# Performance work log

Measured on AMD Instinct MI355X. Metric: run time of the kernel, lower is better.

The kernel has to match this reference:

```python
import jax, jax.numpy as jnp
import numpy as np

NUM_EMBEDDINGS = 1024
EMBEDDING_DIM = 256
COMMITMENT_COST = 0.25
EPS_NORM = 1e-12  # F.normalize eps


def _l2_normalize(x, axis=-1):
    n = jnp.sqrt(jnp.sum(x * x, axis=axis, keepdims=True))
    return x / jnp.maximum(n, EPS_NORM)


def setup_inputs() -> dict:
    key = jax.random.key(0)
    k_in, k_w = jax.random.split(key)
    inputs = jax.random.normal(k_in, (16, 2048, 256), dtype=jnp.float32)
    # nn.Embedding weight initialized uniform(-1/K, 1/K)
    weight = jax.random.uniform(
        k_w, (NUM_EMBEDDINGS, EMBEDDING_DIM), dtype=jnp.float32,
        minval=-1.0 / NUM_EMBEDDINGS, maxval=1.0 / NUM_EMBEDDINGS)
    return {"inputs": inputs, "weight": weight}


def reference(inputs, weight):
    # inputs: [B, T, D]  weight: [K, D]
    B, T, D = inputs.shape
    K = weight.shape[0]

    x = jax.lax.stop_gradient(inputs)
    # cosine distance: normalized dot products  [B, T, K]
    distances = jnp.einsum(
        "btd,kd->btk", _l2_normalize(x), _l2_normalize(weight))

    encoding_indices = jnp.argmax(distances, axis=-1)            # [B, T]
    encodings = jax.nn.one_hot(encoding_indices, K, dtype=jnp.float32)  # [B, T, K]

    # one-hot matmul with codebook == gather
    quantized = jnp.take(weight, encoding_indices, axis=0)       # [B, T, D]

    e_latent_loss = COMMITMENT_COST * jnp.mean(
        (jax.lax.stop_gradient(quantized) - inputs) ** 2)
    q_latent_loss = jnp.mean((quantized - x) ** 2)

    # straight-through estimator
    quantized_st = inputs + jax.lax.stop_gradient(quantized - inputs)

    avg_probs = jnp.mean(encodings, axis=0)                      # [T, K]
    perplexity = jnp.exp(-jnp.sum(avg_probs * jnp.log(avg_probs + 1e-10)))

    # eval path (3D input): contra_loss = 0.0, no EMA/anchor update
    return (quantized_st,
            encoding_indices[..., None],
            q_latent_loss,
            e_latent_loss,
            perplexity,
            encodings)
```

## Files before the change

### kernel.cpp

```cpp
#include <hip/hip_runtime.h>
#include <math.h>
#include <float.h>

#define NUM_EMB   1024
#define DIM       256
#define BATCH     16
#define TLEN      2048
#define NTOK      (BATCH * TLEN)
#define QUANT_N   (NTOK * DIM)

#define QUANT_OFF 0
#define IDX_OFF   QUANT_N
#define QLOSS_OFF (IDX_OFF + NTOK)
#define ELOSS_OFF (QLOSS_OFF + 1)
#define PERP_OFF  (QLOSS_OFF + 2)
#define ENC_OFF   (QLOSS_OFF + 3)

typedef _Float16 f16;
typedef f16   f16x4 __attribute__((ext_vector_type(4)));
typedef f16   f16x8 __attribute__((ext_vector_type(8)));
typedef float f32x4 __attribute__((ext_vector_type(4)));

#define WS_XS_BYTE      0u
#define WS_WSP_BYTE     33554432u
#define WS_CNT_BYTE     34603008u
#define WS_WIN_BYTE     42991616u
#define WS_ACC_BYTE     43253760u
#define WS_NEED         (43253760u + 64u)

#define LWS_WHAT_BYTE   0
#define LWS_CNT_BYTE    1048576
#define LWS_ACC_BYTE    9437184

__device__ __forceinline__ void gl2lds16(const void* g, void* l) {
    __builtin_amdgcn_global_load_lds(
        (const __attribute__((address_space(1))) void*)g,
        (__attribute__((address_space(3))) void*)l, 16, 0, 0);
}


__global__ void k_zero_big(int4* __restrict__ counts4, int4* __restrict__ win4,
                           double* __restrict__ acc) {
    int i = blockIdx.x * blockDim.x + threadIdx.x;
    if (i < 524288) counts4[i] = make_int4(0, 0, 0, 0);
    else            win4[i - 524288] = make_int4(0, 0, 0, 0);
    if (i == 0) { acc[0] = 0.0; acc[1] = 0.0; }
}

__global__ void k_split_x(const float4* __restrict__ x4, f16* __restrict__ Xs) {
    int i = blockIdx.x * 256 + threadIdx.x;
    int row = i >> 6;
    int c4  = i & 63;
    float4 v = x4[i];
    f16 h0 = (f16)v.x, h1 = (f16)v.y, h2 = (f16)v.z, h3 = (f16)v.w;
    f16 l0 = (f16)(v.x - (float)h0), l1 = (f16)(v.y - (float)h1);
    f16 l2 = (f16)(v.z - (float)h2), l3 = (f16)(v.w - (float)h3);
    f16x4 hv = {h0, h1, h2, h3}, lv = {l0, l1, l2, l3};
    *(f16x4*)&Xs[(size_t)row * 512 + c4 * 4]       = hv;
    *(f16x4*)&Xs[(size_t)row * 512 + 256 + c4 * 4] = lv;
}

__global__ void k_norm_w_split(const float* __restrict__ w, f16* __restrict__ Ws) {
    int k = blockIdx.x;
    int lane = threadIdx.x;
    float4 v = ((const float4*)(w + (size_t)k * DIM))[lane];
    float ss = v.x * v.x + v.y * v.y + v.z * v.z + v.w * v.w;
    #pragma unroll
    for (int off = 32; off > 0; off >>= 1) ss += __shfl_down(ss, off);
    ss = __shfl(ss, 0);
    float denom = fmaxf(sqrtf(ss), 1e-12f);
    float a = v.x / denom, b = v.y / denom, c = v.z / denom, d = v.w / denom;
    f16 h0 = (f16)a, h1 = (f16)b, h2 = (f16)c, h3 = (f16)d;
    f16 l0 = (f16)(a - (float)h0), l1 = (f16)(b - (float)h1);
    f16 l2 = (f16)(c - (float)h2), l3 = (f16)(d - (float)h3);
    f16x4 hv = {h0, h1, h2, h3}, lv = {l0, l1, l2, l3};
    *(f16x4*)&Ws[(size_t)k * 512 + lane * 4]       = hv;
    *(f16x4*)&Ws[(size_t)k * 512 + 256 + lane * 4] = lv;
}

__global__ __launch_bounds__(256)
void k_gemm(const f16* __restrict__ Xs,
            const f16* __restrict__ Ws,
            unsigned long long* __restrict__ winners)
{
    __shared__ f16 As[128 * 64];
    __shared__ f16 Bs[128 * 64];

    const int tid  = threadIdx.x;
    const int w    = tid >> 6, lane = tid & 63;
    const int tb   = blockIdx.x & 255;
    const int pg   = blockIdx.x >> 8;
    const int tok0 = tb * 128;
    const int cw0  = pg * 128;
    const int wr   = w >> 1, wc = w & 1;
    const int quad = lane >> 4, l16 = lane & 15;

    const char* Xb = (const char*)Xs + (size_t)tok0 * 1024;
    const char* Wb = (const char*)Ws + (size_t)cw0 * 1024;

    int srow[4], sgpart[4];
    #pragma unroll
    for (int j = 0; j < 4; ++j) {
        int c = (w * 4 + j) * 64 + lane;
        srow[j]   = c >> 3;
        sgpart[j] = ((c & 7) ^ ((c >> 3) & 7)) * 16;
    }

    f32x4 acc[4][4];
    #pragma unroll
    for (int mi = 0; mi < 4; ++mi)
        #pragma unroll
        for (int ni = 0; ni < 4; ++ni)
            acc[mi][ni] = (f32x4){0.f, 0.f, 0.f, 0.f};

    for (int ks = 0; ks < 12; ++ks) {
        const int g = ks >> 2, r = ks & 3;
        const int akoff = ((g == 2) ? 512 : 0) + r * 128;
        const int bkoff = ((g == 1) ? 512 : 0) + r * 128;
        __syncthreads();
        #pragma unroll
        for (int j = 0; j < 4; ++j) {
            gl2lds16(Xb + (size_t)srow[j] * 1024 + akoff + sgpart[j],
                     (char*)As + (w * 4 + j) * 1024);
            gl2lds16(Wb + (size_t)srow[j] * 1024 + bkoff + sgpart[j],
                     (char*)Bs + (w * 4 + j) * 1024);
        }
        __syncthreads();

        #pragma unroll
        for (int ksub = 0; ksub < 2; ++ksub) {
            f16x8 af[4], bf[4];
            #pragma unroll
            for (int mi = 0; mi < 4; ++mi) {
                const int m = wr * 64 + mi * 16 + l16;
                const int slot = (quad + ksub * 4) ^ (l16 & 7);
                af[mi] = *(const f16x8*)&As[m * 64 + slot * 8];
            }
            #pragma unroll
            for (int ni = 0; ni < 4; ++ni) {
                const int n = wc * 64 + ni * 16 + l16;
                const int slot = (quad + ksub * 4) ^ (l16 & 7);
                bf[ni] = *(const f16x8*)&Bs[n * 64 + slot * 8];
            }
            #pragma unroll
            for (int mi = 0; mi < 4; ++mi)
                #pragma unroll
                for (int ni = 0; ni < 4; ++ni)
                    acc[mi][ni] = __builtin_amdgcn_mfma_f32_16x16x32_f16(
                        af[mi], bf[ni], acc[mi][ni], 0, 0, 0);
        }
    }

    #pragma unroll
    for (int mi = 0; mi < 4; ++mi) {
        #pragma unroll
        for (int rr = 0; rr < 4; ++rr) {
            float bv = acc[mi][0][rr];
            int   bk = cw0 + wc * 64 + l16;
            #pragma unroll
            for (int ni = 1; ni < 4; ++ni) {
                float v = acc[mi][ni][rr];
                int  kk = cw0 + wc * 64 + ni * 16 + l16;
                if (v > bv) { bv = v; bk = kk; }
            }
            unsigned int ub = __float_as_uint(bv);
            ub = (ub & 0x80000000u) ? ~ub : (ub | 0x80000000u);
            unsigned long long key =
                ((unsigned long long)ub << 32) | (unsigned int)(1023 - bk);
            #pragma unroll
            for (int msk = 1; msk < 16; msk <<= 1) {
                unsigned long long o = __shfl_xor(key, msk, 64);
                if (o > key) key = o;
            }
            if (l16 == mi * 4 + rr) {
                const int row = wr * 64 + mi * 16 + quad * 4 + rr;
                atomicMax(&winners[tok0 + row], key);
            }
        }
    }
}

__global__ __launch_bounds__(256)
void k_epilogue(const float* __restrict__ x, const float* __restrict__ w,
                const unsigned long long* __restrict__ winners,
                float* __restrict__ out, int* __restrict__ counts,
                double* __restrict__ acc)
{
    const int wv = threadIdx.x >> 6, lane = threadIdx.x & 63;
    const int base = blockIdx.x * 32 + wv * 8;
    float mse = 0.0f;
    for (int t = 0; t < 8; ++t) {
        const int n = base + t;
        const int idx = 1023 - (int)(winners[n] & 1023u);
        float4 wvv = *(const float4*)(w + (size_t)idx * DIM + lane * 4);
        float4 xv  = *(const float4*)(x + (size_t)n * DIM + lane * 4);
        float dx = wvv.x - xv.x, dy = wvv.y - xv.y, dz = wvv.z - xv.z, dw2 = wvv.w - xv.w;
        mse += dx * dx + dy * dy + dz * dz + dw2 * dw2;
        *(float4*)(out + QUANT_OFF + (size_t)n * DIM + lane * 4) = wvv;
        if (lane == 0) {
            out[IDX_OFF + n] = (float)idx;
            atomicAdd(&counts[(n & (TLEN - 1)) * NUM_EMB + idx], 1);
        }
        float* enc = out + ENC_OFF + (size_t)n * NUM_EMB;
        #pragma unroll
        for (int s = 0; s < 4; ++s) {
            int kbase = s * 256 + lane * 4;
            float4 e;
            e.x = (kbase + 0 == idx) ? 1.0f : 0.0f;
            e.y = (kbase + 1 == idx) ? 1.0f : 0.0f;
            e.z = (kbase + 2 == idx) ? 1.0f : 0.0f;
            e.w = (kbase + 3 == idx) ? 1.0f : 0.0f;
            *(float4*)(enc + kbase) = e;
        }
    }
    #pragma unroll
    for (int off = 32; off > 0; off >>= 1) mse += __shfl_down(mse, off);
    if (lane == 0) atomicAdd(&acc[0], (double)mse);
}

__global__ void k_entropy(const int* __restrict__ counts, double* __restrict__ acc) {
    const int tid = blockIdx.x * blockDim.x + threadIdx.x;
    const int stride = gridDim.x * blockDim.x;
    float s = 0.0f;
    for (int e = tid; e < TLEN * NUM_EMB; e += stride) {
        int c = counts[e];
        if (c > 0) {
            float p = (float)c * 0.0625f;
            s += p * logf(p + 1e-10f);
        }
    }
    #pragma unroll
    for (int off = 32; off > 0; off >>= 1) s += __shfl_down(s, off);
    __shared__ float wsum[4];
    int lane = threadIdx.x & 63, wave = threadIdx.x >> 6;
    if (lane == 0) wsum[wave] = s;
    __syncthreads();
    if (threadIdx.x == 0) atomicAdd(&acc[1], (double)(wsum[0] + wsum[1] + wsum[2] + wsum[3]));
}

__global__ void k_final(const double* __restrict__ acc, float* __restrict__ out) {
    float mse_mean = (float)(acc[0] / (double)QUANT_N);
    out[QLOSS_OFF] = mse_mean;
    out[ELOSS_OFF] = 0.25f * mse_mean;
    float arg = -(float)acc[1];
    out[PERP_OFF] = (arg < 87.0f) ? expf(arg) : 3.0e38f;
}

__global__ void k_zero_legacy(int4* __restrict__ counts4, double* __restrict__ acc) {
    int i = blockIdx.x * blockDim.x + threadIdx.x;
    counts4[i] = make_int4(0, 0, 0, 0);
    if (i == 0) { acc[0] = 0.0; acc[1] = 0.0; }
}

__global__ void k_norm_w_legacy(const float* __restrict__ w, float* __restrict__ w_hat) {
    int k = blockIdx.x, lane = threadIdx.x;
    float4 v = ((const float4*)(w + (size_t)k * DIM))[lane];
    float ss = v.x * v.x + v.y * v.y + v.z * v.z + v.w * v.w;
    #pragma unroll
    for (int off = 32; off > 0; off >>= 1) ss += __shfl_down(ss, off);
    ss = __shfl(ss, 0);
    float denom = fmaxf(sqrtf(ss), 1e-12f);
    float4 o = {v.x / denom, v.y / denom, v.z / denom, v.w / denom};
    ((float4*)(w_hat + (size_t)k * DIM))[lane] = o;
}

#define BK 16
#define LDP 132
__global__ __launch_bounds__(256)
void k_main_legacy(const float* __restrict__ x, const float* __restrict__ w,
                   const float* __restrict__ w_hat, float* __restrict__ out,
                   int* __restrict__ counts, double* __restrict__ acc)
{
    __shared__ float As[BK][LDP];
    __shared__ float Bs[BK][LDP];
    __shared__ float redV[128][17];
    __shared__ int   redK[128][17];
    __shared__ int   sIdx[128];

    const int tid  = threadIdx.x;
    const int tok0 = blockIdx.x * 128;
    const int tr   = tid >> 4, tc = tid & 15;
    float rbestV = -3.0e30f; int rbestK = 0;
    const int strow = tid >> 2, stdq = tid & 3;

    for (int panel = 0; panel < 8; ++panel) {
        const int cw0 = panel * 128;
        float accs[8][8];
        #pragma unroll
        for (int i = 0; i < 8; ++i)
            #pragma unroll
            for (int j = 0; j < 8; ++j) accs[i][j] = 0.0f;
        for (int d0 = 0; d0 < DIM; d0 += BK) {
            __syncthreads();
            #pragma unroll
            for (int it = 0; it < 2; ++it) {
                int r = strow + it * 64;
                float4 a = *(const float4*)(x + (size_t)(tok0 + r) * DIM + d0 + stdq * 4);
                float4 b = *(const float4*)(w_hat + (size_t)(cw0 + r) * DIM + d0 + stdq * 4);
                As[stdq * 4 + 0][r] = a.x; As[stdq * 4 + 1][r] = a.y;
                As[stdq * 4 + 2][r] = a.z; As[stdq * 4 + 3][r] = a.w;
                Bs[stdq * 4 + 0][r] = b.x; Bs[stdq * 4 + 1][r] = b.y;
                Bs[stdq * 4 + 2][r] = b.z; Bs[stdq * 4 + 3][r] = b.w;
            }
            __syncthreads();
            #pragma unroll
            for (int kk = 0; kk < BK; ++kk) {
                float4 a0 = *(const float4*)&As[kk][tr * 8];
                float4 a1 = *(const float4*)&As[kk][tr * 8 + 4];
                float4 b0 = *(const float4*)&Bs[kk][tc * 8];
                float4 b1 = *(const float4*)&Bs[kk][tc * 8 + 4];
                float af[8] = {a0.x, a0.y, a0.z, a0.w, a1.x, a1.y, a1.z, a1.w};
                float bf[8] = {b0.x, b0.y, b0.z, b0.w, b1.x, b1.y, b1.z, b1.w};
                #pragma unroll
                for (int i = 0; i < 8; ++i)
                    #pragma unroll
                    for (int j = 0; j < 8; ++j)
                        accs[i][j] = fmaf(af[i], bf[j], accs[i][j]);
            }
        }
        #pragma unroll
        for (int i = 0; i < 8; ++i) {
            float bv = accs[i][0]; int bj = 0;
            #pragma unroll
            for (int j = 1; j < 8; ++j)
                if (accs[i][j] > bv) { bv = accs[i][j]; bj = j; }
            redV[tr * 8 + i][tc] = bv;
            redK[tr * 8 + i][tc] = cw0 + tc * 8 + bj;
        }
        __syncthreads();
        if (tid < 128) {
            #pragma unroll
            for (int g = 0; g < 16; ++g) {
                float v = redV[tid][g]; int kk2 = redK[tid][g];
                if (v > rbestV || (v == rbestV && kk2 < rbestK)) { rbestV = v; rbestK = kk2; }
            }
        }
        __syncthreads();
    }
    if (tid < 128) sIdx[tid] = rbestK;
    __syncthreads();

    const int wave = tid >> 6, lane = tid & 63;
    float mse = 0.0f;
    for (int tl = wave * 32; tl < wave * 32 + 32; ++tl) {
        const int n = tok0 + tl;
        const int idx = sIdx[tl];
        float4 wv = *(const float4*)(w + (size_t)idx * DIM + lane * 4);
        float4 xv = *(const float4*)(x + (size_t)n * DIM + lane * 4);
        float dx = wv.x - xv.x, dy = wv.y - xv.y, dz = wv.z - xv.z, dww = wv.w - xv.w;
        mse += dx * dx + dy * dy + dz * dz + dww * dww;
        *(float4*)(out + QUANT_OFF + (size_t)n * DIM + lane * 4) = wv;
        if (lane == 0) {
            out[IDX_OFF + n] = (float)idx;
            atomicAdd(&counts[(n & (TLEN - 1)) * NUM_EMB + idx], 1);
        }
        float* enc = out + ENC_OFF + (size_t)n * NUM_EMB;
        #pragma unroll
        for (int s = 0; s < 4; ++s) {
            int kbase = s * 256 + lane * 4;
            float4 e;
            e.x = (kbase + 0 == idx) ? 1.0f : 0.0f;
            e.y = (kbase + 1 == idx) ? 1.0f : 0.0f;
            e.z = (kbase + 2 == idx) ? 1.0f : 0.0f;
            e.w = (kbase + 3 == idx) ? 1.0f : 0.0f;
            *(float4*)(enc + kbase) = e;
        }
    }
    #pragma unroll
    for (int off = 32; off > 0; off >>= 1) mse += __shfl_down(mse, off);
    if (lane == 0) atomicAdd(&acc[0], (double)mse);
}

extern "C" void kernel_launch(void* const* d_in, const int* in_sizes, int n_in,
                              void* d_out, int out_size, void* d_ws, size_t ws_size,
                              hipStream_t stream) {
    const float* x = (const float*)d_in[0];
    const float* w = (const float*)d_in[1];
    float* out = (float*)d_out;

    if (ws_size >= WS_NEED) {
        f16*    Xs      = (f16*)((char*)d_ws + WS_XS_BYTE);
        f16*    Wsp     = (f16*)((char*)d_ws + WS_WSP_BYTE);
        int*    counts  = (int*)((char*)d_ws + WS_CNT_BYTE);
        unsigned long long* winners = (unsigned long long*)((char*)d_ws + WS_WIN_BYTE);
        double* acc     = (double*)((char*)d_ws + WS_ACC_BYTE);

        k_zero_big<<<2112, 256, 0, stream>>>((int4*)counts, (int4*)winners, acc);
        k_split_x<<<8192, 256, 0, stream>>>((const float4*)x, Xs);
        k_norm_w_split<<<NUM_EMB, 64, 0, stream>>>(w, Wsp);
        k_gemm<<<2048, 256, 0, stream>>>(Xs, Wsp, winners);
        k_epilogue<<<1024, 256, 0, stream>>>(x, w, winners, out, counts, acc);
        k_entropy<<<512, 256, 0, stream>>>(counts, acc);
        k_final<<<1, 1, 0, stream>>>(acc, out);
    } else {
        float*  w_hat  = (float*)((char*)d_ws + LWS_WHAT_BYTE);
        int*    counts = (int*)((char*)d_ws + LWS_CNT_BYTE);
        double* acc    = (double*)((char*)d_ws + LWS_ACC_BYTE);

        k_zero_legacy<<<2048, 256, 0, stream>>>((int4*)counts, acc);
        k_norm_w_legacy<<<NUM_EMB, 64, 0, stream>>>(w, w_hat);
        k_main_legacy<<<NTOK / 128, 256, 0, stream>>>(x, w, w_hat, out, counts, acc);
        k_entropy<<<512, 256, 0, stream>>>(counts, acc);
        k_final<<<1, 1, 0, stream>>>(acc, out);
    }
}
```

Measured before the change: 335.6 us.

## Fuse prep kernels, double-buffer GEMM LDS, and fuse epilogue via last-block counter

Merges the zeroing, x split and codebook normalize kernels into one launch. The GEMM now double-buffers its LDS tiles so the next k-slice loads while the current one computes. The last of the 8 codebook-group blocks for each token tile, detected through an atomic tile counter, runs the gather, one-hot and loss epilogue inline, which removes a separate epilogue launch. The cost is doubled LDS per block, which can lower occupancy, plus a serialized tail on the last-arriving blocks.

```diff
diff --git a/kernel.cpp b/kernel.cpp
--- a/kernel.cpp
+++ b/kernel.cpp
@@ -26,7 +26,8 @@
 #define WS_CNT_BYTE     34603008u
 #define WS_WIN_BYTE     42991616u
 #define WS_ACC_BYTE     43253760u
-#define WS_NEED         (43253760u + 64u)
+#define WS_TC_BYTE      43253824u
+#define WS_NEED         43254848u
 
 #define LWS_WHAT_BYTE   0
 #define LWS_CNT_BYTE    1048576
@@ -39,127 +40,143 @@
 }
 
 
-__global__ void k_zero_big(int4* __restrict__ counts4, int4* __restrict__ win4,
-                           double* __restrict__ acc) {
-    int i = blockIdx.x * blockDim.x + threadIdx.x;
-    if (i < 524288) counts4[i] = make_int4(0, 0, 0, 0);
-    else            win4[i - 524288] = make_int4(0, 0, 0, 0);
-    if (i == 0) { acc[0] = 0.0; acc[1] = 0.0; }
-}
-
-__global__ void k_split_x(const float4* __restrict__ x4, f16* __restrict__ Xs) {
-    int i = blockIdx.x * 256 + threadIdx.x;
-    int row = i >> 6;
-    int c4  = i & 63;
-    float4 v = x4[i];
-    f16 h0 = (f16)v.x, h1 = (f16)v.y, h2 = (f16)v.z, h3 = (f16)v.w;
-    f16 l0 = (f16)(v.x - (float)h0), l1 = (f16)(v.y - (float)h1);
-    f16 l2 = (f16)(v.z - (float)h2), l3 = (f16)(v.w - (float)h3);
-    f16x4 hv = {h0, h1, h2, h3}, lv = {l0, l1, l2, l3};
-    *(f16x4*)&Xs[(size_t)row * 512 + c4 * 4]       = hv;
-    *(f16x4*)&Xs[(size_t)row * 512 + 256 + c4 * 4] = lv;
-}
-
-__global__ void k_norm_w_split(const float* __restrict__ w, f16* __restrict__ Ws) {
-    int k = blockIdx.x;
-    int lane = threadIdx.x;
-    float4 v = ((const float4*)(w + (size_t)k * DIM))[lane];
-    float ss = v.x * v.x + v.y * v.y + v.z * v.z + v.w * v.w;
-    #pragma unroll
-    for (int off = 32; off > 0; off >>= 1) ss += __shfl_down(ss, off);
-    ss = __shfl(ss, 0);
-    float denom = fmaxf(sqrtf(ss), 1e-12f);
-    float a = v.x / denom, b = v.y / denom, c = v.z / denom, d = v.w / denom;
-    f16 h0 = (f16)a, h1 = (f16)b, h2 = (f16)c, h3 = (f16)d;
-    f16 l0 = (f16)(a - (float)h0), l1 = (f16)(b - (float)h1);
-    f16 l2 = (f16)(c - (float)h2), l3 = (f16)(d - (float)h3);
-    f16x4 hv = {h0, h1, h2, h3}, lv = {l0, l1, l2, l3};
-    *(f16x4*)&Ws[(size_t)k * 512 + lane * 4]       = hv;
-    *(f16x4*)&Ws[(size_t)k * 512 + 256 + lane * 4] = lv;
+__global__ void k_prep(const float4* __restrict__ x4, f16* __restrict__ Xs,
+                       const float* __restrict__ w, f16* __restrict__ Ws,
+                       int4* __restrict__ counts4, int4* __restrict__ win4,
+                       int* __restrict__ tilecnt, double* __restrict__ acc)
+{
+    const int b = blockIdx.x, tid = threadIdx.x;
+    if (b < 8192) {
+        int i = b * 256 + tid;
+        int row = i >> 6, c4 = i & 63;
+        float4 v = x4[i];
+        f16 h0 = (f16)v.x, h1 = (f16)v.y, h2 = (f16)v.z, h3 = (f16)v.w;
+        f16 l0 = (f16)(v.x - (float)h0), l1 = (f16)(v.y - (float)h1);
+        f16 l2 = (f16)(v.z - (float)h2), l3 = (f16)(v.w - (float)h3);
+        f16x4 hv = {h0, h1, h2, h3}, lv = {l0, l1, l2, l3};
+        *(f16x4*)&Xs[(size_t)row * 512 + c4 * 4]       = hv;
+        *(f16x4*)&Xs[(size_t)row * 512 + 256 + c4 * 4] = lv;
+    } else if (b < 10240) {
+        counts4[(b - 8192) * 256 + tid] = make_int4(0, 0, 0, 0);
+    } else if (b < 10304) {
+        win4[(b - 10240) * 256 + tid] = make_int4(0, 0, 0, 0);
+    } else if (b < 10560) {
+        int k = (b - 10304) * 4 + (tid >> 6);
+        int lane = tid & 63;
+        float4 v = ((const float4*)(w + (size_t)k * DIM))[lane];
+        float ss = v.x * v.x + v.y * v.y + v.z * v.z + v.w * v.w;
+        #pragma unroll
+        for (int off = 32; off > 0; off >>= 1) ss += __shfl_down(ss, off);
+        ss = __shfl(ss, 0);
+        float denom = fmaxf(sqrtf(ss), 1e-12f);
+        float a = v.x / denom, bb = v.y / denom, c = v.z / denom, d = v.w / denom;
+        f16 h0 = (f16)a, h1 = (f16)bb, h2 = (f16)c, h3 = (f16)d;
+        f16 l0 = (f16)(a - (float)h0), l1 = (f16)(bb - (float)h1);
+        f16 l2 = (f16)(c - (float)h2), l3 = (f16)(d - (float)h3);
+        f16x4 hv = {h0, h1, h2, h3}, lv = {l0, l1, l2, l3};
+        *(f16x4*)&Ws[(size_t)k * 512 + lane * 4]       = hv;
+        *(f16x4*)&Ws[(size_t)k * 512 + 256 + lane * 4] = lv;
+    } else {
+        if (tid < 256) tilecnt[tid] = 0;
+        if (tid == 0) { acc[0] = 0.0; acc[1] = 0.0; }
+    }
 }
 
 __global__ __launch_bounds__(256)
 void k_gemm(const f16* __restrict__ Xs,
             const f16* __restrict__ Ws,
-            unsigned long long* __restrict__ winners)
+            const float* __restrict__ x, const float* __restrict__ w,
+            unsigned long long* __restrict__ winners,
+            int* __restrict__ counts, int* __restrict__ tilecnt,
+            float* __restrict__ out, double* __restrict__ acc)
 {
-    __shared__ f16 As[128 * 64];
-    __shared__ f16 Bs[128 * 64];
+    __shared__ f16 A0[8192];
+    __shared__ f16 B0[8192];
+    __shared__ f16 A1[8192];
+    __shared__ f16 B1[8192];
+    __shared__ int sLast;
 
     const int tid  = threadIdx.x;
-    const int w    = tid >> 6, lane = tid & 63;
+    const int wv   = tid >> 6, lane = tid & 63;
     const int tb   = blockIdx.x & 255;
     const int pg   = blockIdx.x >> 8;
     const int tok0 = tb * 128;
     const int cw0  = pg * 128;
-    const int wr   = w >> 1, wc = w & 1;
+    const int wr   = wv >> 1, wc = wv & 1;
     const int quad = lane >> 4, l16 = lane & 15;
 
     const char* Xb = (const char*)Xs + (size_t)tok0 * 1024;
     const char* Wb = (const char*)Ws + (size_t)cw0 * 1024;
 
-    int srow[4], sgpart[4];
+    int srow[4], sgoff[4];
     #pragma unroll
     for (int j = 0; j < 4; ++j) {
-        int c = (w * 4 + j) * 64 + lane;
-        srow[j]   = c >> 3;
-        sgpart[j] = ((c & 7) ^ ((c >> 3) & 7)) * 16;
-    }
-
-    f32x4 acc[4][4];
+        int c = (wv * 4 + j) * 64 + lane;
+        srow[j] = c >> 3;
+        sgoff[j] = ((c & 7) ^ ((c >> 3) & 7)) * 16;
+    }
+    const int ldsbase = wv * 4096;
+
+    f32x4 acc4[4][4];
     #pragma unroll
     for (int mi = 0; mi < 4; ++mi)
         #pragma unroll
         for (int ni = 0; ni < 4; ++ni)
-            acc[mi][ni] = (f32x4){0.f, 0.f, 0.f, 0.f};
-
-    for (int ks = 0; ks < 12; ++ks) {
+            acc4[mi][ni] = (f32x4){0.f, 0.f, 0.f, 0.f};
+
+    auto stage = [&](int ks, f16* Ad, f16* Bd) {
         const int g = ks >> 2, r = ks & 3;
-        const int akoff = ((g == 2) ? 512 : 0) + r * 128;
-        const int bkoff = ((g == 1) ? 512 : 0) + r * 128;
-        __syncthreads();
+        const int ak = ((g == 2) ? 512 : 0) + r * 128;
+        const int bk = ((g == 1) ? 512 : 0) + r * 128;
         #pragma unroll
         for (int j = 0; j < 4; ++j) {
-            gl2lds16(Xb + (size_t)srow[j] * 1024 + akoff + sgpart[j],
-                     (char*)As + (w * 4 + j) * 1024);
-            gl2lds16(Wb + (size_t)srow[j] * 1024 + bkoff + sgpart[j],
-                     (char*)Bs + (w * 4 + j) * 1024);
-        }
-        __syncthreads();
-
+            gl2lds16(Xb + (size_t)srow[j] * 1024 + ak + sgoff[j],
+                     (char*)Ad + ldsbase + j * 1024);
+            gl2lds16(Wb + (size_t)srow[j] * 1024 + bk + sgoff[j],
+                     (char*)Bd + ldsbase + j * 1024);
+        }
+    };
+    auto compute = [&](const f16* Ab, const f16* Bb) {
         #pragma unroll
         for (int ksub = 0; ksub < 2; ++ksub) {
+            const int slot = ((quad + ksub * 4) ^ (l16 & 7)) * 8;
             f16x8 af[4], bf[4];
             #pragma unroll
-            for (int mi = 0; mi < 4; ++mi) {
-                const int m = wr * 64 + mi * 16 + l16;
-                const int slot = (quad + ksub * 4) ^ (l16 & 7);
-                af[mi] = *(const f16x8*)&As[m * 64 + slot * 8];
-            }
-            #pragma unroll
-            for (int ni = 0; ni < 4; ++ni) {
-                const int n = wc * 64 + ni * 16 + l16;
-                const int slot = (quad + ksub * 4) ^ (l16 & 7);
-                bf[ni] = *(const f16x8*)&Bs[n * 64 + slot * 8];
-            }
+            for (int mi = 0; mi < 4; ++mi)
+                af[mi] = *(const f16x8*)&Ab[(wr * 64 + mi * 16 + l16) * 64 + slot];
+            #pragma unroll
+            for (int ni = 0; ni < 4; ++ni)
+                bf[ni] = *(const f16x8*)&Bb[(wc * 64 + ni * 16 + l16) * 64 + slot];
             #pragma unroll
             for (int mi = 0; mi < 4; ++mi)
                 #pragma unroll
                 for (int ni = 0; ni < 4; ++ni)
-                    acc[mi][ni] = __builtin_amdgcn_mfma_f32_16x16x32_f16(
-                        af[mi], bf[ni], acc[mi][ni], 0, 0, 0);
-        }
+                    acc4[mi][ni] = __builtin_amdgcn_mfma_f32_16x16x32_f16(
+                        af[mi], bf[ni], acc4[mi][ni], 0, 0, 0);
+        }
+    };
+
+    stage(0, A0, B0);
+    __syncthreads();
+    #pragma unroll
+    for (int ks = 0; ks < 12; ks += 2) {
+        stage(ks + 1, A1, B1);
+        compute(A0, B0);
+        __syncthreads();
+        if (ks < 10) stage(ks + 2, A0, B0);
+        compute(A1, B1);
+        __syncthreads();
     }
 
     #pragma unroll
     for (int mi = 0; mi < 4; ++mi) {
         #pragma unroll
         for (int rr = 0; rr < 4; ++rr) {
-            float bv = acc[mi][0][rr];
+            float bv = acc4[mi][0][rr];
             int   bk = cw0 + wc * 64 + l16;
             #pragma unroll
             for (int ni = 1; ni < 4; ++ni) {
-                float v = acc[mi][ni][rr];
+                float v = acc4[mi][ni][rr];
                 int  kk = cw0 + wc * 64 + ni * 16 + l16;
                 if (v > bv) { bv = v; bk = kk; }
             }
@@ -178,20 +195,19 @@
             }
         }
     }
-}
-
-__global__ __launch_bounds__(256)
-void k_epilogue(const float* __restrict__ x, const float* __restrict__ w,
-                const unsigned long long* __restrict__ winners,
-                float* __restrict__ out, int* __restrict__ counts,
-                double* __restrict__ acc)
-{
-    const int wv = threadIdx.x >> 6, lane = threadIdx.x & 63;
-    const int base = blockIdx.x * 32 + wv * 8;
+
+    __threadfence();
+    __syncthreads();
+    if (tid == 0) sLast = (atomicAdd(&tilecnt[tb], 1) == 7) ? 1 : 0;
+    __syncthreads();
+    if (!sLast) return;
+
+    unsigned long long myk = 0;
+    if (lane < 32) myk = atomicMax(&winners[tok0 + wv * 32 + lane], 0ull);
     float mse = 0.0f;
-    for (int t = 0; t < 8; ++t) {
-        const int n = base + t;
-        const int idx = 1023 - (int)(winners[n] & 1023u);
+    for (int t = 0; t < 32; ++t) {
+        const int n = tok0 + wv * 32 + t;
+        const int idx = 1023 - (int)(__shfl(myk, t, 64) & 1023u);
         float4 wvv = *(const float4*)(w + (size_t)idx * DIM + lane * 4);
         float4 xv  = *(const float4*)(x + (size_t)n * DIM + lane * 4);
         float dx = wvv.x - xv.x, dy = wvv.y - xv.y, dz = wvv.z - xv.z, dw2 = wvv.w - xv.w;
@@ -384,12 +400,12 @@
         int*    counts  = (int*)((char*)d_ws + WS_CNT_BYTE);
         unsigned long long* winners = (unsigned long long*)((char*)d_ws + WS_WIN_BYTE);
         double* acc     = (double*)((char*)d_ws + WS_ACC_BYTE);
-
-        k_zero_big<<<2112, 256, 0, stream>>>((int4*)counts, (int4*)winners, acc);
-        k_split_x<<<8192, 256, 0, stream>>>((const float4*)x, Xs);
-        k_norm_w_split<<<NUM_EMB, 64, 0, stream>>>(w, Wsp);
-        k_gemm<<<2048, 256, 0, stream>>>(Xs, Wsp, winners);
-        k_epilogue<<<1024, 256, 0, stream>>>(x, w, winners, out, counts, acc);
+        int*    tilecnt = (int*)((char*)d_ws + WS_TC_BYTE);
+
+        k_prep<<<10561, 256, 0, stream>>>((const float4*)x, Xs, w, Wsp,
+                                          (int4*)counts, (int4*)winners, tilecnt, acc);
+        k_gemm<<<2048, 256, 0, stream>>>(Xs, Wsp, x, w, winners, counts, tilecnt,
+                                         out, acc);
         k_entropy<<<512, 256, 0, stream>>>(counts, acc);
         k_final<<<1, 1, 0, stream>>>(acc, out);
     } else {
```

After: 396.7 us. 18.2% more time.

## Fuse prep kernels and double-buffer a larger 256x128 GEMM tile

Applied to the files above, without the earlier changes.

Merges the zeroing, x-split and weight-normalize kernels into one prep launch to cut launch overhead. The GEMM tile grows to 256 tokens by 128 codes with 32-wide K steps. LDS is double-buffered so the next stage's global-to-LDS loads overlap the current MFMA work, and one barrier per step replaces two. This raises register use (acc[8][4]) under launch bounds of 2 blocks per SM and changes the LDS swizzle, which risks spills or bank conflicts.

```diff
diff --git a/kernel.cpp b/kernel.cpp
--- a/kernel.cpp
+++ b/kernel.cpp
@@ -39,120 +39,134 @@
 }
 
 
-__global__ void k_zero_big(int4* __restrict__ counts4, int4* __restrict__ win4,
-                           double* __restrict__ acc) {
-    int i = blockIdx.x * blockDim.x + threadIdx.x;
-    if (i < 524288) counts4[i] = make_int4(0, 0, 0, 0);
-    else            win4[i - 524288] = make_int4(0, 0, 0, 0);
-    if (i == 0) { acc[0] = 0.0; acc[1] = 0.0; }
-}
-
-__global__ void k_split_x(const float4* __restrict__ x4, f16* __restrict__ Xs) {
-    int i = blockIdx.x * 256 + threadIdx.x;
-    int row = i >> 6;
-    int c4  = i & 63;
-    float4 v = x4[i];
-    f16 h0 = (f16)v.x, h1 = (f16)v.y, h2 = (f16)v.z, h3 = (f16)v.w;
-    f16 l0 = (f16)(v.x - (float)h0), l1 = (f16)(v.y - (float)h1);
-    f16 l2 = (f16)(v.z - (float)h2), l3 = (f16)(v.w - (float)h3);
-    f16x4 hv = {h0, h1, h2, h3}, lv = {l0, l1, l2, l3};
-    *(f16x4*)&Xs[(size_t)row * 512 + c4 * 4]       = hv;
-    *(f16x4*)&Xs[(size_t)row * 512 + 256 + c4 * 4] = lv;
-}
-
-__global__ void k_norm_w_split(const float* __restrict__ w, f16* __restrict__ Ws) {
-    int k = blockIdx.x;
-    int lane = threadIdx.x;
-    float4 v = ((const float4*)(w + (size_t)k * DIM))[lane];
-    float ss = v.x * v.x + v.y * v.y + v.z * v.z + v.w * v.w;
-    #pragma unroll
-    for (int off = 32; off > 0; off >>= 1) ss += __shfl_down(ss, off);
-    ss = __shfl(ss, 0);
-    float denom = fmaxf(sqrtf(ss), 1e-12f);
-    float a = v.x / denom, b = v.y / denom, c = v.z / denom, d = v.w / denom;
-    f16 h0 = (f16)a, h1 = (f16)b, h2 = (f16)c, h3 = (f16)d;
-    f16 l0 = (f16)(a - (float)h0), l1 = (f16)(b - (float)h1);
-    f16 l2 = (f16)(c - (float)h2), l3 = (f16)(d - (float)h3);
-    f16x4 hv = {h0, h1, h2, h3}, lv = {l0, l1, l2, l3};
-    *(f16x4*)&Ws[(size_t)k * 512 + lane * 4]       = hv;
-    *(f16x4*)&Ws[(size_t)k * 512 + 256 + lane * 4] = lv;
-}
-
-__global__ __launch_bounds__(256)
+__global__ void k_prep(const float4* __restrict__ x4, f16* __restrict__ Xs,
+                       const float* __restrict__ w, f16* __restrict__ Ws,
+                       int4* __restrict__ counts4, int4* __restrict__ win4,
+                       double* __restrict__ acc)
+{
+    const int b = blockIdx.x, tid = threadIdx.x;
+    if (b < 8192) {
+        int i = b * 256 + tid;
+        int row = i >> 6, c4 = i & 63;
+        float4 v = x4[i];
+        f16 h0 = (f16)v.x, h1 = (f16)v.y, h2 = (f16)v.z, h3 = (f16)v.w;
+        f16 l0 = (f16)(v.x - (float)h0), l1 = (f16)(v.y - (float)h1);
+        f16 l2 = (f16)(v.z - (float)h2), l3 = (f16)(v.w - (float)h3);
+        f16x4 hv = {h0, h1, h2, h3}, lv = {l0, l1, l2, l3};
+        *(f16x4*)&Xs[(size_t)row * 512 + c4 * 4]       = hv;
+        *(f16x4*)&Xs[(size_t)row * 512 + 256 + c4 * 4] = lv;
+    } else if (b < 10240) {
+        counts4[(b - 8192) * 256 + tid] = make_int4(0, 0, 0, 0);
+    } else if (b < 10304) {
+        win4[(b - 10240) * 256 + tid] = make_int4(0, 0, 0, 0);
+        if (b == 10240 && tid == 0) { acc[0] = 0.0; acc[1] = 0.0; }
+    } else {
+        int k = (b - 10304) * 4 + (tid >> 6);
+        int lane = tid & 63;
+        float4 v = ((const float4*)(w + (size_t)k * DIM))[lane];
+        float ss = v.x * v.x + v.y * v.y + v.z * v.z + v.w * v.w;
+        #pragma unroll
+        for (int off = 32; off > 0; off >>= 1) ss += __shfl_down(ss, off);
+        ss = __shfl(ss, 0);
+        float denom = fmaxf(sqrtf(ss), 1e-12f);
+        float a = v.x / denom, bb = v.y / denom, c = v.z / denom, d = v.w / denom;
+        f16 h0 = (f16)a, h1 = (f16)bb, h2 = (f16)c, h3 = (f16)d;
+        f16 l0 = (f16)(a - (float)h0), l1 = (f16)(bb - (float)h1);
+        f16 l2 = (f16)(c - (float)h2), l3 = (f16)(d - (float)h3);
+        f16x4 hv = {h0, h1, h2, h3}, lv = {l0, l1, l2, l3};
+        *(f16x4*)&Ws[(size_t)k * 512 + lane * 4]       = hv;
+        *(f16x4*)&Ws[(size_t)k * 512 + 256 + lane * 4] = lv;
+    }
+}
+
+__global__ __launch_bounds__(256, 2)
 void k_gemm(const f16* __restrict__ Xs,
             const f16* __restrict__ Ws,
             unsigned long long* __restrict__ winners)
 {
-    __shared__ f16 As[128 * 64];
-    __shared__ f16 Bs[128 * 64];
+    __shared__ char As[2][16384];
+    __shared__ char Bs[2][8192];
 
     const int tid  = threadIdx.x;
-    const int w    = tid >> 6, lane = tid & 63;
-    const int tb   = blockIdx.x & 255;
-    const int pg   = blockIdx.x >> 8;
-    const int tok0 = tb * 128;
+    const int wv   = tid >> 6, lane = tid & 63;
+    const int tb   = blockIdx.x & 127;
+    const int pg   = blockIdx.x >> 7;
+    const int tok0 = tb * 256;
     const int cw0  = pg * 128;
-    const int wr   = w >> 1, wc = w & 1;
+    const int wr   = wv >> 1, wc = wv & 1;
     const int quad = lane >> 4, l16 = lane & 15;
 
     const char* Xb = (const char*)Xs + (size_t)tok0 * 1024;
     const char* Wb = (const char*)Ws + (size_t)cw0 * 1024;
 
-    int srow[4], sgpart[4];
+    int rA[4], qA[4], rB[2], qB[2];
     #pragma unroll
     for (int j = 0; j < 4; ++j) {
-        int c = (w * 4 + j) * 64 + lane;
-        srow[j]   = c >> 3;
-        sgpart[j] = ((c & 7) ^ ((c >> 3) & 7)) * 16;
-    }
-
-    f32x4 acc[4][4];
-    #pragma unroll
-    for (int mi = 0; mi < 4; ++mi)
+        int c = j * 256 + wv * 64 + lane;
+        rA[j] = c >> 2;
+        qA[j] = ((c & 3) ^ ((c >> 4) & 3)) * 16;
+    }
+    #pragma unroll
+    for (int j = 0; j < 2; ++j) {
+        int c = j * 256 + wv * 64 + lane;
+        rB[j] = c >> 2;
+        qB[j] = ((c & 3) ^ ((c >> 4) & 3)) * 16;
+    }
+
+    f32x4 acc[8][4];
+    #pragma unroll
+    for (int mi = 0; mi < 8; ++mi)
         #pragma unroll
         for (int ni = 0; ni < 4; ++ni)
             acc[mi][ni] = (f32x4){0.f, 0.f, 0.f, 0.f};
 
-    for (int ks = 0; ks < 12; ++ks) {
-        const int g = ks >> 2, r = ks & 3;
-        const int akoff = ((g == 2) ? 512 : 0) + r * 128;
-        const int bkoff = ((g == 1) ? 512 : 0) + r * 128;
+    auto stage = [&](int ks, int buf) {
+        const int g = ks >> 3, r8 = ks & 7;
+        const int ak = ((g == 2) ? 512 : 0) + r8 * 64;
+        const int bk = ((g == 1) ? 512 : 0) + r8 * 64;
+        #pragma unroll
+        for (int j = 0; j < 4; ++j)
+            gl2lds16(Xb + (size_t)rA[j] * 1024 + ak + qA[j],
+                     &As[buf][(j * 256 + wv * 64) * 16]);
+        #pragma unroll
+        for (int j = 0; j < 2; ++j)
+            gl2lds16(Wb + (size_t)rB[j] * 1024 + bk + qB[j],
+                     &Bs[buf][(j * 256 + wv * 64) * 16]);
+    };
+
+    const int slotoff = ((quad ^ (l16 >> 2)) & 3) * 16;
+
+    auto compute = [&](int buf) {
+        f16x8 af[8], bf[4];
+        #pragma unroll
+        for (int mi = 0; mi < 8; ++mi) {
+            const int row = wr * 128 + mi * 16 + l16;
+            af[mi] = *(const f16x8*)&As[buf][row * 64 + slotoff];
+        }
+        #pragma unroll
+        for (int ni = 0; ni < 4; ++ni) {
+            const int row = wc * 64 + ni * 16 + l16;
+            bf[ni] = *(const f16x8*)&Bs[buf][row * 64 + slotoff];
+        }
+        #pragma unroll
+        for (int mi = 0; mi < 8; ++mi)
+            #pragma unroll
+            for (int ni = 0; ni < 4; ++ni)
+                acc[mi][ni] = __builtin_amdgcn_mfma_f32_16x16x32_f16(
+                    af[mi], bf[ni], acc[mi][ni], 0, 0, 0);
+    };
+
+    stage(0, 0);
+    __syncthreads();
+    #pragma unroll
+    for (int ks = 0; ks < 24; ++ks) {
+        if (ks < 23) stage(ks + 1, (ks + 1) & 1);
+        compute(ks & 1);
         __syncthreads();
-        #pragma unroll
-        for (int j = 0; j < 4; ++j) {
-            gl2lds16(Xb + (size_t)srow[j] * 1024 + akoff + sgpart[j],
-                     (char*)As + (w * 4 + j) * 1024);
-            gl2lds16(Wb + (size_t)srow[j] * 1024 + bkoff + sgpart[j],
-                     (char*)Bs + (w * 4 + j) * 1024);
-        }
-        __syncthreads();
-
-        #pragma unroll
-        for (int ksub = 0; ksub < 2; ++ksub) {
-            f16x8 af[4], bf[4];
-            #pragma unroll
-            for (int mi = 0; mi < 4; ++mi) {
-                const int m = wr * 64 + mi * 16 + l16;
-                const int slot = (quad + ksub * 4) ^ (l16 & 7);
-                af[mi] = *(const f16x8*)&As[m * 64 + slot * 8];
-            }
-            #pragma unroll
-            for (int ni = 0; ni < 4; ++ni) {
-                const int n = wc * 64 + ni * 16 + l16;
-                const int slot = (quad + ksub * 4) ^ (l16 & 7);
-                bf[ni] = *(const f16x8*)&Bs[n * 64 + slot * 8];
-            }
-            #pragma unroll
-            for (int mi = 0; mi < 4; ++mi)
-                #pragma unroll
-                for (int ni = 0; ni < 4; ++ni)
-                    acc[mi][ni] = __builtin_amdgcn_mfma_f32_16x16x32_f16(
-                        af[mi], bf[ni], acc[mi][ni], 0, 0, 0);
-        }
-    }
-
-    #pragma unroll
-    for (int mi = 0; mi < 4; ++mi) {
+    }
+
+    #pragma unroll
+    for (int mi = 0; mi < 8; ++mi) {
         #pragma unroll
         for (int rr = 0; rr < 4; ++rr) {
             float bv = acc[mi][0][rr];
@@ -172,8 +186,8 @@
                 unsigned long long o = __shfl_xor(key, msk, 64);
                 if (o > key) key = o;
             }
-            if (l16 == mi * 4 + rr) {
-                const int row = wr * 64 + mi * 16 + quad * 4 + rr;
+            if (l16 == ((mi * 4 + rr) & 15)) {
+                const int row = wr * 128 + mi * 16 + quad * 4 + rr;
                 atomicMax(&winners[tok0 + row], key);
             }
         }
@@ -385,10 +399,9 @@
         unsigned long long* winners = (unsigned long long*)((char*)d_ws + WS_WIN_BYTE);
         double* acc     = (double*)((char*)d_ws + WS_ACC_BYTE);
 
-        k_zero_big<<<2112, 256, 0, stream>>>((int4*)counts, (int4*)winners, acc);
-        k_split_x<<<8192, 256, 0, stream>>>((const float4*)x, Xs);
-        k_norm_w_split<<<NUM_EMB, 64, 0, stream>>>(w, Wsp);
-        k_gemm<<<2048, 256, 0, stream>>>(Xs, Wsp, winners);
+        k_prep<<<10560, 256, 0, stream>>>((const float4*)x, Xs, w, Wsp,
+                                          (int4*)counts, (int4*)winners, acc);
+        k_gemm<<<1024, 256, 0, stream>>>(Xs, Wsp, winners);
         k_epilogue<<<1024, 256, 0, stream>>>(x, w, winners, out, counts, acc);
         k_entropy<<<512, 256, 0, stream>>>(counts, acc);
         k_final<<<1, 1, 0, stream>>>(acc, out);
```

New measurement: 329.9 us. Within noise of the previous version (-1.7%).
